# Kernel tuning notes

Measured on AMD Instinct MI355X. Metric: run time of the kernel, lower is better.

## Reference

```python
import jax, jax.numpy as jnp
import numpy as np


def setup_inputs() -> dict:
    key = jax.random.key(0)
    ks = jax.random.split(key, 16)
    B, P, ENC = 128, 196, 2048          # batch, num pixels (14x14), encoder feature size
    E = D = A = 512                      # embed, decoder(hidden), attention sizes
    V, L = 10000, 52                     # vocab, max caption length
    s = 0.02
    rn = lambda k, shp: jax.random.normal(k, shp, jnp.float32) * s
    return {
        "features": jax.random.normal(ks[0], (B, P, ENC), jnp.float32),
        "captions": jax.random.randint(ks[1], (B, L), 0, V),
        "caption_lengths": jax.random.randint(ks[2], (B, 1), 2, L + 1),
        "emb": jax.random.uniform(ks[3], (V, E), jnp.float32, -0.1, 0.1),
        "W_enc_att": rn(ks[4], (ENC, A)), "b_enc_att": jnp.zeros((A,), jnp.float32),
        "W_dec_att": rn(ks[5], (D, A)),   "b_dec_att": jnp.zeros((A,), jnp.float32),
        "w_full": rn(ks[6], (A,)),        "b_full": jnp.zeros((), jnp.float32),
        "W_h0": rn(ks[7], (ENC, D)),      "b_h0": jnp.zeros((D,), jnp.float32),
        "W_c0": rn(ks[8], (ENC, D)),      "b_c0": jnp.zeros((D,), jnp.float32),
        "W_beta": rn(ks[9], (D, ENC)),    "b_beta": jnp.zeros((ENC,), jnp.float32),
        "W_ih": rn(ks[10], (E + ENC, 4 * D)), "b_ih": jnp.zeros((4 * D,), jnp.float32),
        "W_hh": rn(ks[11], (D, 4 * D)),       "b_hh": jnp.zeros((4 * D,), jnp.float32),
        "W_fc": jax.random.uniform(ks[12], (D, V), jnp.float32, -0.1, 0.1),
        "b_fc": jnp.zeros((V,), jnp.float32),
    }


def reference(features, captions, caption_lengths, emb,
              W_enc_att, b_enc_att, W_dec_att, b_dec_att, w_full, b_full,
              W_h0, b_h0, W_c0, b_c0, W_beta, b_beta,
              W_ih, b_ih, W_hh, b_hh, W_fc, b_fc):
    lens = caption_lengths[:, 0]
    order = jnp.argsort(-lens)                       # sort descending by length (stable)
    features = features[order]
    captions = captions[order]
    decode_lengths = lens[order] - 1                 # [B]
    T = captions.shape[1] - 1                        # static max decode length

    emb_seq = emb[captions[:, :T]]                   # [B,T,E]
    eo = features.mean(axis=1)                       # [B,ENC]
    h = eo @ W_h0 + b_h0                             # [B,D]
    c = eo @ W_c0 + b_c0
    enc_proj = features @ W_enc_att + b_enc_att      # [B,P,A] (precomputed, h-independent)

    def step(carry, xs):
        h, c = carry
        t, e_t = xs                                  # e_t: [B,E]
        mask = (decode_lengths > t)[:, None].astype(h.dtype)  # rows still decoding
        dec_proj = h @ W_dec_att + b_dec_att         # [B,A]
        scores = jax.nn.relu(enc_proj + dec_proj[:, None, :]) @ w_full + b_full  # [B,P]
        alpha = jax.nn.softmax(scores, axis=-1)      # [B,P]
        attw = jnp.einsum('bp,bpe->be', alpha, features)       # attention-weighted enc
        gate = jax.nn.sigmoid(h @ W_beta + b_beta)   # [B,ENC]
        x = jnp.concatenate([e_t, gate * attw], axis=1)        # [B,E+ENC]
        gates = x @ W_ih + b_ih + h @ W_hh + b_hh    # [B,4D], torch LSTMCell order i,f,g,o
        i, f, g, o = jnp.split(gates, 4, axis=1)
        c_new = jax.nn.sigmoid(f) * c + jax.nn.sigmoid(i) * jnp.tanh(g)
        h_new = jax.nn.sigmoid(o) * jnp.tanh(c_new)
        preds = h_new @ W_fc + b_fc                  # dropout is identity in eval
        h = mask * h_new + (1.0 - mask) * h          # freeze finished rows
        c = mask * c_new + (1.0 - mask) * c
        return (h, c), (preds * mask, alpha * mask)

    (_, _), (preds, alphas) = jax.lax.scan(
        step, (h, c), (jnp.arange(T), jnp.swapaxes(emb_seq, 0, 1)))
    predictions = jnp.swapaxes(preds, 0, 1)          # [B,T,V]
    alphas = jnp.swapaxes(alphas, 0, 1)              # [B,T,P]
    return predictions, captions, decode_lengths, alphas
```

## Files before the change

### kernel.cpp

```cpp
#include <hip/hip_runtime.h>
#include <math.h>

#define NB 128
#define NP 196
#define NENC 2048
#define NE 512
#define ND 512
#define NA 512
#define NV 10000
#define NVPAD 10112
#define NL 52
#define NT 51
#define KXH2 2560

typedef unsigned short u16;
typedef __attribute__((ext_vector_type(8))) short bf16x8;
typedef __attribute__((ext_vector_type(8))) unsigned short u16x8;
typedef __attribute__((ext_vector_type(4))) float f32x4;

#define MFMA16 __builtin_amdgcn_mfma_f32_16x16x32_bf16

__device__ __forceinline__ float sigmoidf_(float v) { return 1.0f / (1.0f + __expf(-v)); }
__device__ __forceinline__ float b2f(u16 u) { return __uint_as_float(((unsigned int)u) << 16); }
__device__ __forceinline__ u16 f2b(float f) {
  unsigned int u = __float_as_uint(f);
  unsigned int r = (u + 0x7FFFu + ((u >> 16) & 1u)) >> 16;
  return (u16)r;
}

__global__ void kSort(const int* __restrict__ cap_len, const int* __restrict__ captions,
                      int* __restrict__ order, int* __restrict__ nact,
                      float* __restrict__ out_cap, float* __restrict__ out_dlen) {
  __shared__ int lens[NB];
  __shared__ int s_dl[NB];
  int tid = threadIdx.x;
  lens[tid] = cap_len[tid];
  __syncthreads();
  int li = lens[tid];
  int r = 0;
  for (int j = 0; j < NB; ++j) {
    int lj = lens[j];
    if (lj > li || (lj == li && j < tid)) r++;
  }
  order[r] = tid;
  s_dl[r] = li - 1;
  out_dlen[r] = (float)(li - 1);
  for (int l = 0; l < NL; ++l)
    out_cap[(size_t)r * NL + l] = (float)captions[(size_t)tid * NL + l];
  __syncthreads();
  if (tid < NT) {
    int cnt = 0;
    for (int j = 0; j < NB; ++j) cnt += (s_dl[j] > tid) ? 1 : 0;
    nact[tid] = cnt;
  }
}

__global__ void kAlphaZero(const int* __restrict__ nact, float* __restrict__ out_alph) {
  int t = blockIdx.x;
  int n0 = nact[t];
  int cnt = (NB - n0) * NP;
  for (int i = threadIdx.x; i < cnt; i += 256) {
    int b = n0 + i / NP;
    int p = i - (i / NP) * NP;
    out_alph[((size_t)b * NT + t) * NP + p] = 0.0f;
  }
}

__global__ void kFeats(const float* __restrict__ features, const int* __restrict__ order,
                       u16* __restrict__ featsb) {
  int p = blockIdx.x, b = blockIdx.y, tid = threadIdx.x;
  const float* src = features + ((size_t)order[b] * NP + p) * NENC + tid * 8;
  u16* dst = featsb + ((size_t)b * NP + p) * NENC + tid * 8;
  float4 v0 = *(const float4*)src;
  float4 v1 = *(const float4*)(src + 4);
  u16x8 o;
  o[0] = f2b(v0.x); o[1] = f2b(v0.y); o[2] = f2b(v0.z); o[3] = f2b(v0.w);
  o[4] = f2b(v1.x); o[5] = f2b(v1.y); o[6] = f2b(v1.z); o[7] = f2b(v1.w);
  *(u16x8*)dst = o;
}

__global__ void kTWenc(const float* __restrict__ W, u16* __restrict__ dst) {
  int n = blockIdx.x;
  for (int k = threadIdx.x; k < NENC; k += 256)
    dst[(size_t)n * NENC + k] = f2b(W[(size_t)k * NA + n]);
}
__global__ void kTdg(const float* __restrict__ Wdec, const float* __restrict__ Wbeta,
                     u16* __restrict__ dst) {
  int n = blockIdx.x;
  for (int k = threadIdx.x; k < ND; k += 256) {
    float v = (n < NA) ? Wdec[(size_t)k * NA + n] : Wbeta[(size_t)k * NENC + (n - NA)];
    dst[(size_t)n * ND + k] = f2b(v);
  }
}
__global__ void kTWihTop(const float* __restrict__ Wih, u16* __restrict__ dst) {
  int n = blockIdx.x;
  int col = (n & 3) * ND + (n >> 2);
  for (int k = threadIdx.x; k < NE; k += 256)
    dst[(size_t)n * NE + k] = f2b(Wih[(size_t)k * (4 * ND) + col]);
}
__global__ void kTifgo2(const float* __restrict__ Wih, const float* __restrict__ Whh,
                        u16* __restrict__ dst) {
  int n = blockIdx.x;
  int col = (n & 3) * ND + (n >> 2);
  for (int k = threadIdx.x; k < KXH2; k += 256) {
    float v = (k < NENC) ? Wih[(size_t)(NE + k) * (4 * ND) + col]
                         : Whh[(size_t)(k - NENC) * (4 * ND) + col];
    dst[(size_t)n * KXH2 + k] = f2b(v);
  }
}
__global__ void kTfc(const float* __restrict__ Wfc, u16* __restrict__ dst) {
  int n = blockIdx.x;
  for (int k = threadIdx.x; k < ND; k += 256) {
    float v = (n < NV) ? Wfc[(size_t)k * NV + n] : 0.0f;
    dst[(size_t)n * ND + k] = f2b(v);
  }
}

__global__ void kEmbA(const float* __restrict__ emb, const int* __restrict__ captions,
                      const int* __restrict__ order, u16* __restrict__ embA) {
  int t = blockIdx.x, b = blockIdx.y;
  int tok = captions[(size_t)order[b] * NL + t];
  int i = threadIdx.x * 2;
  float2 v = *(const float2*)(emb + (size_t)tok * NE + i);
  unsigned int w0 = (unsigned int)f2b(v.x) | ((unsigned int)f2b(v.y) << 16);
  *(unsigned int*)(embA + ((size_t)t * NB + b) * NE + i) = w0;
}

__global__ __launch_bounds__(256) void kEmbGemm(const u16* __restrict__ A,
                                                const u16* __restrict__ BT,
                                                u16* __restrict__ D) {
  int w = threadIdx.x >> 6, lane = threadIdx.x & 63;
  int lr = lane & 15, lg = lane >> 4;
  int mb = blockIdx.y * 128 + w * 32;
  int nb = blockIdx.x * 64;
  f32x4 acc[2][4] = {};
  const u16* a0 = A + (size_t)(mb + lr) * NE + lg * 8;
  const u16* a1 = a0 + 16 * NE;
  const u16* b0 = BT + (size_t)(nb + lr) * NE + lg * 8;
  for (int k0 = 0; k0 < NE; k0 += 32) {
    bf16x8 af0 = *(const bf16x8*)(a0 + k0);
    bf16x8 af1 = *(const bf16x8*)(a1 + k0);
#pragma unroll
    for (int nt = 0; nt < 4; ++nt) {
      bf16x8 bf = *(const bf16x8*)(b0 + (size_t)nt * 16 * NE + k0);
      acc[0][nt] = MFMA16(af0, bf, acc[0][nt], 0, 0, 0);
      acc[1][nt] = MFMA16(af1, bf, acc[1][nt], 0, 0, 0);
    }
  }
#pragma unroll
  for (int mt = 0; mt < 2; ++mt)
#pragma unroll
    for (int nt = 0; nt < 4; ++nt)
#pragma unroll
      for (int j = 0; j < 4; ++j) {
        int row = mb + mt * 16 + lg * 4 + j;
        int col = nb + nt * 16 + lr;
        D[(size_t)row * NENC + col] = f2b(acc[mt][nt][j]);
      }
}

__global__ void kEo(const u16* __restrict__ featsb, float* __restrict__ eo) {
  int e = blockIdx.x * 256 + threadIdx.x;
  int b = blockIdx.y;
  const u16* f = featsb + (size_t)b * NP * NENC + e;
  float s = 0.0f;
  for (int p = 0; p < NP; ++p) s += b2f(f[(size_t)p * NENC]);
  eo[(size_t)b * NENC + e] = s * (1.0f / NP);
}

__global__ void kInitHC(const float* __restrict__ eo,
                        const float* __restrict__ W_h0, const float* __restrict__ b_h0,
                        const float* __restrict__ W_c0, const float* __restrict__ b_c0,
                        u16* __restrict__ hb, u16* __restrict__ xh0, float* __restrict__ c) {
  __shared__ float s_eo[NENC];
  int b = blockIdx.y;
  for (int i = threadIdx.x; i < NENC; i += 256) s_eo[i] = eo[(size_t)b * NENC + i];
  __syncthreads();
  int d = blockIdx.x * 256 + threadIdx.x;
  const float* W = blockIdx.z ? W_c0 : W_h0;
  const float* bias = blockIdx.z ? b_c0 : b_h0;
  float acc = bias[d];
  for (int k = 0; k < NENC; ++k) acc += s_eo[k] * W[(size_t)k * ND + d];
  if (blockIdx.z) {
    c[(size_t)b * ND + d] = acc;
  } else {
    u16 hv = f2b(acc);
    hb[(size_t)b * ND + d] = hv;
    xh0[(size_t)b * KXH2 + NENC + d] = hv;
  }
}

__global__ __launch_bounds__(256) void kEncProj(const u16* __restrict__ A,
                                                const u16* __restrict__ BT,
                                                const float* __restrict__ bias,
                                                u16* __restrict__ D) {
  __shared__ u16 As[128][72];
  int bid = blockIdx.x;
  int mt = bid >> 2, ntile = bid & 3;
  int mb = mt * 128, nb = ntile * 128;
  int tid = threadIdx.x;
  int w = tid >> 6, lane = tid & 63;
  int lr = lane & 15, lg = lane >> 4;

  int arow[4], akp[4];
  const u16* aptr[4];
#pragma unroll
  for (int i = 0; i < 4; ++i) {
    int idx = i * 256 + tid;
    arow[i] = idx >> 3;
    akp[i] = idx & 7;
    aptr[i] = A + (size_t)(mb + arow[i]) * NENC + akp[i] * 8;
  }
  u16x8 stg0, stg1, stg2, stg3;
  stg0 = *(const u16x8*)(aptr[0]);
  stg1 = *(const u16x8*)(aptr[1]);
  stg2 = *(const u16x8*)(aptr[2]);
  stg3 = *(const u16x8*)(aptr[3]);

  f32x4 acc[2][8] = {};
  const u16* bbase = BT + (size_t)(nb + lr) * NENC + lg * 8;

  for (int k0 = 0; k0 < NENC; k0 += 64) {
    __syncthreads();
    *(u16x8*)&As[arow[0]][akp[0] * 8] = stg0;
    *(u16x8*)&As[arow[1]][akp[1] * 8] = stg1;
    *(u16x8*)&As[arow[2]][akp[2] * 8] = stg2;
    *(u16x8*)&As[arow[3]][akp[3] * 8] = stg3;
    if (k0 + 64 < NENC) {
      stg0 = *(const u16x8*)(aptr[0] + k0 + 64);
      stg1 = *(const u16x8*)(aptr[1] + k0 + 64);
      stg2 = *(const u16x8*)(aptr[2] + k0 + 64);
      stg3 = *(const u16x8*)(aptr[3] + k0 + 64);
    }
    __syncthreads();
#pragma unroll
    for (int kh = 0; kh < 2; ++kh) {
      int r0 = w * 32 + lr;
      bf16x8 af0 = *(const bf16x8*)&As[r0][kh * 32 + lg * 8];
      bf16x8 af1 = *(const bf16x8*)&As[r0 + 16][kh * 32 + lg * 8];
#pragma unroll
      for (int nt = 0; nt < 8; ++nt) {
        bf16x8 bf = *(const bf16x8*)(bbase + (size_t)nt * 16 * NENC + k0 + kh * 32);
        acc[0][nt] = MFMA16(af0, bf, acc[0][nt], 0, 0, 0);
        acc[1][nt] = MFMA16(af1, bf, acc[1][nt], 0, 0, 0);
      }
    }
  }
#pragma unroll
  for (int m2 = 0; m2 < 2; ++m2)
#pragma unroll
    for (int nt = 0; nt < 8; ++nt)
#pragma unroll
      for (int j = 0; j < 4; ++j) {
        int row = mb + w * 32 + m2 * 16 + lg * 4 + j;
        int col = nb + nt * 16 + lr;
        D[(size_t)row * NA + col] = f2b(acc[m2][nt][j] + bias[col]);
      }
}

__global__ __launch_bounds__(64) void kDecGate(const u16* __restrict__ hb,
                                               const u16* __restrict__ BT,
                                               const float* __restrict__ b_dec,
                                               const float* __restrict__ b_beta,
                                               const int* __restrict__ nact, int t,
                                               float* __restrict__ dec_proj,
                                               float* __restrict__ gate_raw) {
  int nact_t = nact[t];
  int mb = blockIdx.y * 32;
  if (mb >= nact_t) return;
  int lane = threadIdx.x;
  int lr = lane & 15, lg = lane >> 4;
  int nb = blockIdx.x * 32;
  f32x4 acc[2][2] = {};
  const u16* a0 = hb + (size_t)(mb + lr) * ND + lg * 8;
  const u16* a1 = a0 + 16 * ND;
  const u16* b0 = BT + (size_t)(nb + lr) * ND + lg * 8;
  const u16* b1 = b0 + 16 * ND;
#pragma unroll 4
  for (int k0 = 0; k0 < ND; k0 += 32) {
    bf16x8 af0 = *(const bf16x8*)(a0 + k0);
    bf16x8 af1 = *(const bf16x8*)(a1 + k0);
    bf16x8 bv0 = *(const bf16x8*)(b0 + k0);
    bf16x8 bv1 = *(const bf16x8*)(b1 + k0);
    acc[0][0] = MFMA16(af0, bv0, acc[0][0], 0, 0, 0);
    acc[1][0] = MFMA16(af1, bv0, acc[1][0], 0, 0, 0);
    acc[0][1] = MFMA16(af0, bv1, acc[0][1], 0, 0, 0);
    acc[1][1] = MFMA16(af1, bv1, acc[1][1], 0, 0, 0);
  }
#pragma unroll
  for (int mt = 0; mt < 2; ++mt)
#pragma unroll
    for (int nt = 0; nt < 2; ++nt)
#pragma unroll
      for (int j = 0; j < 4; ++j) {
        int row = mb + mt * 16 + lg * 4 + j;
        int n = nb + nt * 16 + lr;
        if (n < NA)
          dec_proj[(size_t)row * NA + n] = acc[mt][nt][j] + b_dec[n];
        else
          gate_raw[(size_t)row * NENC + (n - NA)] = acc[mt][nt][j] + b_beta[n - NA];
      }
}

__global__ __launch_bounds__(256) void kSAX(const u16* __restrict__ featsb,
                                            const u16* __restrict__ encb,
                                            const float* __restrict__ dec_proj,
                                            const float* __restrict__ gate_raw,
                                            const float* __restrict__ w_full,
                                            const float* __restrict__ b_full,
                                            const int* __restrict__ nact, int t,
                                            u16* __restrict__ xh_w,
                                            float* __restrict__ out_alph) {
  int b = blockIdx.x, r = blockIdx.y, tid = threadIdx.x;
  if (b >= nact[t]) return;
  __shared__ float s_dp[NA], s_wf[NA], s_al[NP + 12], red[16];
  for (int i = tid; i < NA; i += 256) { s_dp[i] = dec_proj[(size_t)b * NA + i]; s_wf[i] = w_full[i]; }
  __syncthreads();
  int wave = tid >> 6, lane = tid & 63;
  float bf_ = b_full[0];
  for (int p = wave; p < NP; p += 4) {
    const u16* ep = encb + ((size_t)b * NP + p) * NA + lane * 8;
    u16x8 v = *(const u16x8*)ep;
    float acc = 0.0f;
#pragma unroll
    for (int j = 0; j < 8; ++j) {
      int a = lane * 8 + j;
      float vv = b2f(v[j]) + s_dp[a];
      acc += fmaxf(vv, 0.0f) * s_wf[a];
    }
#pragma unroll
    for (int off = 32; off; off >>= 1) acc += __shfl_down(acc, off);
    if (lane == 0) s_al[p] = acc + bf_;
  }
  __syncthreads();
  float mx = -3.4e38f;
  for (int p = tid; p < NP; p += 256) mx = fmaxf(mx, s_al[p]);
#pragma unroll
  for (int off = 32; off; off >>= 1) mx = fmaxf(mx, __shfl_down(mx, off));
  if (lane == 0) red[wave] = mx;
  __syncthreads();
  if (tid == 0) red[0] = fmaxf(fmaxf(red[0], red[1]), fmaxf(red[2], red[3]));
  __syncthreads();
  float m2v = red[0];
  float sm = 0.0f;
  for (int p = tid; p < NP; p += 256) { float e = __expf(s_al[p] - m2v); s_al[p] = e; sm += e; }
#pragma unroll
  for (int off = 32; off; off >>= 1) sm += __shfl_down(sm, off);
  if (lane == 0) red[8 + wave] = sm;
  __syncthreads();
  if (tid == 0) red[8] = 1.0f / (red[8] + red[9] + red[10] + red[11]);
  __syncthreads();
  float inv = red[8];
  for (int p = tid; p < NP; p += 256) {
    float al = s_al[p] * inv;
    s_al[p] = al;
    if (r == 0) out_alph[((size_t)b * NT + t) * NP + p] = al;
  }
  __syncthreads();
  int e0 = r * 512 + tid * 2;
  float ac0 = 0.0f, ac1 = 0.0f;
  const u16* fb = featsb + (size_t)b * NP * NENC + e0;
#pragma unroll 4
  for (int p = 0; p < NP; ++p) {
    unsigned int v = *(const unsigned int*)(fb + (size_t)p * NENC);
    float al = s_al[p];
    ac0 += al * __uint_as_float(v << 16);
    ac1 += al * __uint_as_float(v & 0xffff0000u);
  }
  float g0 = sigmoidf_(gate_raw[(size_t)b * NENC + e0]);
  float g1 = sigmoidf_(gate_raw[(size_t)b * NENC + e0 + 1]);
  unsigned int wo = (unsigned int)f2b(ac0 * g0) | ((unsigned int)f2b(ac1 * g1) << 16);
  *(unsigned int*)(xh_w + (size_t)b * KXH2 + e0) = wo;
}

__global__ __launch_bounds__(1024) void kGatesLstm(const u16* __restrict__ xh_r,
                                                   const u16* __restrict__ WifgoT2,
                                                   const u16* __restrict__ embAll,
                                                   const float* __restrict__ b_ih,
                                                   const float* __restrict__ b_hh,
                                                   const int* __restrict__ nact, int t,
                                                   float* __restrict__ cst,
                                                   u16* __restrict__ hb,
                                                   u16* __restrict__ hnewAll_t,
                                                   u16* __restrict__ xh_w) {
  __shared__ float smem[8 * 32 * 33];
  int nact_t = nact[t];
  int tid = threadIdx.x;
  int w = tid >> 6, lane = tid & 63;
  int lr = lane & 15, lg = lane >> 4;
  int rt = blockIdx.x & 3, ct = blockIdx.x >> 2;
  int mb = rt * 32, nb = ct * 32;
  int kq = w >> 1, mh = w & 1;
  if (mb < nact_t) {
    f32x4 acc0 = {}, acc1 = {};
    const u16* pa = xh_r + (size_t)(mb + mh * 16 + lr) * KXH2 + kq * 320 + lg * 8;
    const u16* pb0 = WifgoT2 + (size_t)(nb + lr) * KXH2 + kq * 320 + lg * 8;
    const u16* pb1 = pb0 + (size_t)16 * KXH2;
#pragma unroll
    for (int k0 = 0; k0 < 320; k0 += 32) {
      bf16x8 af = *(const bf16x8*)(pa + k0);
      bf16x8 bv0 = *(const bf16x8*)(pb0 + k0);
      bf16x8 bv1 = *(const bf16x8*)(pb1 + k0);
      acc0 = MFMA16(af, bv0, acc0, 0, 0, 0);
      acc1 = MFMA16(af, bv1, acc1, 0, 0, 0);
    }
#pragma unroll
    for (int j = 0; j < 4; ++j) {
      int rr = kq * 32 + mh * 16 + lg * 4 + j;
      smem[rr * 33 + lr] = acc0[j];
      smem[rr * 33 + 16 + lr] = acc1[j];
    }
  }
  __syncthreads();
  if (tid < 256) {
    int row = tid >> 3, dl = tid & 7;
    int grow = mb + row;
    int d = ct * 8 + dl;
    size_t off = (size_t)grow * ND + d;
    if (grow < nact_t) {
      float g4[4];
#pragma unroll
      for (int g = 0; g < 4; ++g) {
        int col = dl * 4 + g;
        float s = 0.0f;
#pragma unroll
        for (int q = 0; q < 8; ++q) s += smem[(q * 32 + row) * 33 + col];
        s += b2f(embAll[((size_t)t * NB + grow) * NENC + nb + col]);
        g4[g] = s;
      }
      float gi = g4[0] + b_ih[d] + b_hh[d];
      float gf = g4[1] + b_ih[ND + d] + b_hh[ND + d];
      float gg = g4[2] + b_ih[2 * ND + d] + b_hh[2 * ND + d];
      float go = g4[3] + b_ih[3 * ND + d] + b_hh[3 * ND + d];
      float cn = sigmoidf_(gf) * cst[off] + sigmoidf_(gi) * tanhf(gg);
      float hn = sigmoidf_(go) * tanhf(cn);
      u16 hv = f2b(hn);
      cst[off] = cn;
      hb[off] = hv;
      hnewAll_t[off] = hv;
      xh_w[(size_t)grow * KXH2 + NENC + d] = hv;
    } else {
      xh_w[(size_t)grow * KXH2 + NENC + d] = hb[off];
    }
  }
}

__global__ __launch_bounds__(256) void kPredsAllT(const u16* __restrict__ hnewAll,
                                                  const u16* __restrict__ BT,
                                                  const float* __restrict__ b_fc,
                                                  const int* __restrict__ nact,
                                                  float* __restrict__ out_pred) {
  int nb = blockIdx.x * 64;
  int w = threadIdx.x >> 6, lane = threadIdx.x & 63;
  int lr = lane & 15, lg = lane >> 4;
  int mb = w * 32;
  const u16* b0 = BT + (size_t)(nb + lr) * ND + lg * 8;
#pragma unroll
  for (int ti = 0; ti < 4; ++ti) {
    int t = blockIdx.y * 4 + ti;
    if (t >= NT) break;
    int nact_t = nact[t];
    f32x4 acc[2][4] = {};
    if (mb < nact_t) {
      const u16* a0 = hnewAll + (size_t)t * NB * ND + (size_t)(mb + lr) * ND + lg * 8;
      const u16* a1 = a0 + 16 * ND;
      for (int k0 = 0; k0 < ND; k0 += 32) {
        bf16x8 af0 = *(const bf16x8*)(a0 + k0);
        bf16x8 af1 = *(const bf16x8*)(a1 + k0);
#pragma unroll
        for (int nt = 0; nt < 4; ++nt) {
          bf16x8 bf = *(const bf16x8*)(b0 + (size_t)nt * 16 * ND + k0);
          acc[0][nt] = MFMA16(af0, bf, acc[0][nt], 0, 0, 0);
          acc[1][nt] = MFMA16(af1, bf, acc[1][nt], 0, 0, 0);
        }
      }
    }
#pragma unroll
    for (int mt = 0; mt < 2; ++mt)
#pragma unroll
      for (int nt = 0; nt < 4; ++nt)
#pragma unroll
        for (int j = 0; j < 4; ++j) {
          int gn = nb + nt * 16 + lr;
          if (gn < NV) {
            int row = mb + mt * 16 + lg * 4 + j;
            float v = (row < nact_t) ? (acc[mt][nt][j] + b_fc[gn]) : 0.0f;
            __builtin_nontemporal_store(v, &out_pred[((size_t)row * NT + t) * NV + gn]);
          }
        }
  }
}

extern "C" void kernel_launch(void* const* d_in, const int* in_sizes, int n_in,
                              void* d_out, int out_size, void* d_ws, size_t ws_size,
                              hipStream_t stream) {
  (void)in_sizes; (void)n_in; (void)out_size; (void)ws_size;
  const float* features  = (const float*)d_in[0];
  const int*   captions  = (const int*)d_in[1];
  const int*   cap_len   = (const int*)d_in[2];
  const float* emb       = (const float*)d_in[3];
  const float* W_enc_att = (const float*)d_in[4];
  const float* b_enc_att = (const float*)d_in[5];
  const float* W_dec_att = (const float*)d_in[6];
  const float* b_dec_att = (const float*)d_in[7];
  const float* w_full    = (const float*)d_in[8];
  const float* b_full    = (const float*)d_in[9];
  const float* W_h0      = (const float*)d_in[10];
  const float* b_h0      = (const float*)d_in[11];
  const float* W_c0      = (const float*)d_in[12];
  const float* b_c0      = (const float*)d_in[13];
  const float* W_beta    = (const float*)d_in[14];
  const float* b_beta    = (const float*)d_in[15];
  const float* W_ih      = (const float*)d_in[16];
  const float* b_ih      = (const float*)d_in[17];
  const float* W_hh      = (const float*)d_in[18];
  const float* b_hh      = (const float*)d_in[19];
  const float* W_fc      = (const float*)d_in[20];
  const float* b_fc      = (const float*)d_in[21];

  float* out      = (float*)d_out;
  float* out_pred = out;
  float* out_cap  = out_pred + (size_t)NB * NT * NV;
  float* out_dlen = out_cap + (size_t)NB * NL;
  float* out_alph = out_dlen + NB;

  char* p = (char*)d_ws;
  auto alloc = [&](size_t nbytes) { void* r = (void*)p; p += (nbytes + 255) & ~(size_t)255; return r; };
  int*   order    = (int*)alloc(NB * 4);
  int*   nact     = (int*)alloc(NT * 4);
  float* eo       = (float*)alloc((size_t)NB * NENC * 4);
  float* c        = (float*)alloc((size_t)NB * ND * 4);
  u16*   hb       = (u16*)alloc((size_t)NB * ND * 2);
  u16*   xh0      = (u16*)alloc((size_t)NB * KXH2 * 2);
  u16*   xh1      = (u16*)alloc((size_t)NB * KXH2 * 2);
  u16*   hnewAll  = (u16*)alloc((size_t)NT * NB * ND * 2);
  float* dec_proj = (float*)alloc((size_t)NB * NA * 4);
  float* gate_raw = (float*)alloc((size_t)NB * NENC * 4);
  u16*   featsb   = (u16*)alloc((size_t)NB * NP * NENC * 2);
  u16*   encb     = (u16*)alloc((size_t)NB * NP * NA * 2);
  u16*   WencT    = (u16*)alloc((size_t)NA * NENC * 2);
  u16*   WdgT     = (u16*)alloc((size_t)(NA + NENC) * ND * 2);
  u16*   WihTopT  = (u16*)alloc((size_t)NENC * NE * 2);
  u16*   WifgoT2  = (u16*)alloc((size_t)NENC * KXH2 * 2);
  u16*   WfcT     = (u16*)alloc((size_t)NVPAD * ND * 2);
  u16*   embA     = (u16*)alloc((size_t)NT * NB * NE * 2);
  u16*   embAll   = (u16*)alloc((size_t)NT * NB * NENC * 2);

  kSort<<<1, NB, 0, stream>>>(cap_len, captions, order, nact, out_cap, out_dlen);
  kAlphaZero<<<NT, 256, 0, stream>>>(nact, out_alph);
  kFeats<<<dim3(NP, NB), 256, 0, stream>>>(features, order, featsb);
  kTWenc<<<NA, 256, 0, stream>>>(W_enc_att, WencT);
  kTdg<<<NA + NENC, 256, 0, stream>>>(W_dec_att, W_beta, WdgT);
  kTWihTop<<<NENC, 256, 0, stream>>>(W_ih, WihTopT);
  kTifgo2<<<NENC, 256, 0, stream>>>(W_ih, W_hh, WifgoT2);
  kTfc<<<NVPAD, 256, 0, stream>>>(W_fc, WfcT);
  kEmbA<<<dim3(NT, NB), 256, 0, stream>>>(emb, captions, order, embA);
  kEmbGemm<<<dim3(NENC / 64, NT), 256, 0, stream>>>(embA, WihTopT, embAll);
  kEo<<<dim3(NENC / 256, NB), 256, 0, stream>>>(featsb, eo);
  kInitHC<<<dim3(ND / 256, NB, 2), 256, 0, stream>>>(eo, W_h0, b_h0, W_c0, b_c0, hb, xh0, c);
  kEncProj<<<784, 256, 0, stream>>>(featsb, WencT, b_enc_att, encb);

  for (int t = 0; t < NT; ++t) {
    u16* xh_r = (t & 1) ? xh1 : xh0;
    u16* xh_w = (t & 1) ? xh0 : xh1;
    kDecGate<<<dim3((NA + NENC) / 32, 4), 64, 0, stream>>>(hb, WdgT, b_dec_att, b_beta,
                                                           nact, t, dec_proj, gate_raw);
    kSAX<<<dim3(NB, 4), 256, 0, stream>>>(featsb, encb, dec_proj, gate_raw, w_full, b_full,
                                          nact, t, xh_r, out_alph);
    kGatesLstm<<<256, 1024, 0, stream>>>(xh_r, WifgoT2, embAll, b_ih, b_hh, nact, t,
                                         c, hb, hnewAll + (size_t)t * NB * ND, xh_w);
  }
  kPredsAllT<<<dim3(NVPAD / 64, (NT + 3) / 4), 256, 0, stream>>>(hnewAll, WfcT, b_fc, nact, out_pred);
}
```

Before: 4.618 ms.

## Tile weight transposes, MFMA init-state GEMM, double-buffer enc proj, reshape preds grid

The separate per-row weight transpose kernels become one LDS-tiled transpose kernel with coalesced reads and vectorised writes. The scalar fp32 h0/c0 initialisation becomes a bf16 MFMA GEMM against a new transposed combined W_h0/W_c0 matrix. The encoder projection GEMM double-buffers its LDS A tile so each k-step needs one barrier instead of two. The prediction kernel launches one block per timestep and vocab tile instead of looping over four timesteps, which gives more blocks. The cost is extra workspace and bf16 rounding of the mean feature vector and of the init weights.

```diff
diff --git a/kernel.cpp b/kernel.cpp
--- a/kernel.cpp
+++ b/kernel.cpp
@@ -79,41 +79,43 @@
   *(u16x8*)dst = o;
 }
 
-__global__ void kTWenc(const float* __restrict__ W, u16* __restrict__ dst) {
-  int n = blockIdx.x;
-  for (int k = threadIdx.x; k < NENC; k += 256)
-    dst[(size_t)n * NENC + k] = f2b(W[(size_t)k * NA + n]);
-}
-__global__ void kTdg(const float* __restrict__ Wdec, const float* __restrict__ Wbeta,
-                     u16* __restrict__ dst) {
-  int n = blockIdx.x;
-  for (int k = threadIdx.x; k < ND; k += 256) {
-    float v = (n < NA) ? Wdec[(size_t)k * NA + n] : Wbeta[(size_t)k * NENC + (n - NA)];
-    dst[(size_t)n * ND + k] = f2b(v);
-  }
-}
-__global__ void kTWihTop(const float* __restrict__ Wih, u16* __restrict__ dst) {
-  int n = blockIdx.x;
-  int col = (n & 3) * ND + (n >> 2);
-  for (int k = threadIdx.x; k < NE; k += 256)
-    dst[(size_t)n * NE + k] = f2b(Wih[(size_t)k * (4 * ND) + col]);
-}
-__global__ void kTifgo2(const float* __restrict__ Wih, const float* __restrict__ Whh,
-                        u16* __restrict__ dst) {
-  int n = blockIdx.x;
-  int col = (n & 3) * ND + (n >> 2);
-  for (int k = threadIdx.x; k < KXH2; k += 256) {
-    float v = (k < NENC) ? Wih[(size_t)(NE + k) * (4 * ND) + col]
-                         : Whh[(size_t)(k - NENC) * (4 * ND) + col];
-    dst[(size_t)n * KXH2 + k] = f2b(v);
-  }
-}
-__global__ void kTfc(const float* __restrict__ Wfc, u16* __restrict__ dst) {
-  int n = blockIdx.x;
-  for (int k = threadIdx.x; k < ND; k += 256) {
-    float v = (n < NV) ? Wfc[(size_t)k * NV + n] : 0.0f;
-    dst[(size_t)n * ND + k] = f2b(v);
-  }
+__device__ __forceinline__ float tfetch(int mode, int k, int n,
+                                        const float* __restrict__ A,
+                                        const float* __restrict__ B) {
+  switch (mode) {
+    case 0: return A[(size_t)k * NA + n];
+    case 1: return (n < NA) ? A[(size_t)k * NA + n] : B[(size_t)k * NENC + (n - NA)];
+    case 2: return A[(size_t)k * (4 * ND) + (n & 3) * ND + (n >> 2)];
+    case 3: {
+      int col = (n & 3) * ND + (n >> 2);
+      return (k < NENC) ? A[(size_t)(NE + k) * (4 * ND) + col]
+                        : B[(size_t)(k - NENC) * (4 * ND) + col];
+    }
+    case 4: return (n < NV) ? A[(size_t)k * NV + n] : 0.0f;
+    default: return (n < NA) ? A[(size_t)k * ND + n] : B[(size_t)k * ND + (n - NA)];
+  }
+}
+
+__global__ __launch_bounds__(256) void kTrans(const float* __restrict__ A,
+                                              const float* __restrict__ B,
+                                              u16* __restrict__ dst,
+                                              int K, int N, int mode) {
+  __shared__ u16 T[32][136];
+  int n0 = blockIdx.x * 32, k0 = blockIdx.y * 128;
+  int tid = threadIdx.x;
+  int c = tid & 31, kr = tid >> 5;
+#pragma unroll
+  for (int pass = 0; pass < 16; ++pass) {
+    int kl = pass * 8 + kr;
+    T[c][kl] = f2b(tfetch(mode, k0 + kl, n0 + c, A, B));
+  }
+  __syncthreads();
+  int row = tid >> 3, seg = tid & 7;
+  u16x8 v0, v1;
+#pragma unroll
+  for (int j = 0; j < 8; ++j) { v0[j] = T[row][seg * 16 + j]; v1[j] = T[row][seg * 16 + 8 + j]; }
+  *(u16x8*)&dst[(size_t)(n0 + row) * K + k0 + seg * 16] = v0;
+  *(u16x8*)&dst[(size_t)(n0 + row) * K + k0 + seg * 16 + 8] = v1;
 }
 
 __global__ void kEmbA(const float* __restrict__ emb, const int* __restrict__ captions,
@@ -159,42 +161,63 @@
       }
 }
 
-__global__ void kEo(const u16* __restrict__ featsb, float* __restrict__ eo) {
+__global__ void kEo(const u16* __restrict__ featsb, u16* __restrict__ eob) {
   int e = blockIdx.x * 256 + threadIdx.x;
   int b = blockIdx.y;
   const u16* f = featsb + (size_t)b * NP * NENC + e;
   float s = 0.0f;
   for (int p = 0; p < NP; ++p) s += b2f(f[(size_t)p * NENC]);
-  eo[(size_t)b * NENC + e] = s * (1.0f / NP);
-}
-
-__global__ void kInitHC(const float* __restrict__ eo,
-                        const float* __restrict__ W_h0, const float* __restrict__ b_h0,
-                        const float* __restrict__ W_c0, const float* __restrict__ b_c0,
-                        u16* __restrict__ hb, u16* __restrict__ xh0, float* __restrict__ c) {
-  __shared__ float s_eo[NENC];
-  int b = blockIdx.y;
-  for (int i = threadIdx.x; i < NENC; i += 256) s_eo[i] = eo[(size_t)b * NENC + i];
-  __syncthreads();
-  int d = blockIdx.x * 256 + threadIdx.x;
-  const float* W = blockIdx.z ? W_c0 : W_h0;
-  const float* bias = blockIdx.z ? b_c0 : b_h0;
-  float acc = bias[d];
-  for (int k = 0; k < NENC; ++k) acc += s_eo[k] * W[(size_t)k * ND + d];
-  if (blockIdx.z) {
-    c[(size_t)b * ND + d] = acc;
-  } else {
-    u16 hv = f2b(acc);
-    hb[(size_t)b * ND + d] = hv;
-    xh0[(size_t)b * KXH2 + NENC + d] = hv;
-  }
+  eob[(size_t)b * NENC + e] = f2b(s * (1.0f / NP));
+}
+
+__global__ __launch_bounds__(64) void kHC0(const u16* __restrict__ eob,
+                                           const u16* __restrict__ BT,
+                                           const float* __restrict__ b_h0,
+                                           const float* __restrict__ b_c0,
+                                           u16* __restrict__ hb, u16* __restrict__ xh0,
+                                           float* __restrict__ c) {
+  int lane = threadIdx.x;
+  int lr = lane & 15, lg = lane >> 4;
+  int mb = blockIdx.y * 32, nb = blockIdx.x * 32;
+  f32x4 acc[2][2] = {};
+  const u16* a0 = eob + (size_t)(mb + lr) * NENC + lg * 8;
+  const u16* a1 = a0 + 16 * NENC;
+  const u16* b0 = BT + (size_t)(nb + lr) * NENC + lg * 8;
+  const u16* b1 = b0 + 16 * NENC;
+#pragma unroll 4
+  for (int k0 = 0; k0 < NENC; k0 += 32) {
+    bf16x8 af0 = *(const bf16x8*)(a0 + k0);
+    bf16x8 af1 = *(const bf16x8*)(a1 + k0);
+    bf16x8 bv0 = *(const bf16x8*)(b0 + k0);
+    bf16x8 bv1 = *(const bf16x8*)(b1 + k0);
+    acc[0][0] = MFMA16(af0, bv0, acc[0][0], 0, 0, 0);
+    acc[1][0] = MFMA16(af1, bv0, acc[1][0], 0, 0, 0);
+    acc[0][1] = MFMA16(af0, bv1, acc[0][1], 0, 0, 0);
+    acc[1][1] = MFMA16(af1, bv1, acc[1][1], 0, 0, 0);
+  }
+#pragma unroll
+  for (int mt = 0; mt < 2; ++mt)
+#pragma unroll
+    for (int nt = 0; nt < 2; ++nt)
+#pragma unroll
+      for (int j = 0; j < 4; ++j) {
+        int row = mb + mt * 16 + lg * 4 + j;
+        int n = nb + nt * 16 + lr;
+        if (n < NA) {
+          u16 hv = f2b(acc[mt][nt][j] + b_h0[n]);
+          hb[(size_t)row * ND + n] = hv;
+          xh0[(size_t)row * KXH2 + NENC + n] = hv;
+        } else {
+          c[(size_t)row * ND + (n - NA)] = acc[mt][nt][j] + b_c0[n - NA];
+        }
+      }
 }
 
 __global__ __launch_bounds__(256) void kEncProj(const u16* __restrict__ A,
                                                 const u16* __restrict__ BT,
                                                 const float* __restrict__ bias,
                                                 u16* __restrict__ D) {
-  __shared__ u16 As[128][72];
+  __shared__ u16 As[2][128][72];
   int bid = blockIdx.x;
   int mt = bid >> 2, ntile = bid & 3;
   int mb = mt * 128, nb = ntile * 128;
@@ -211,33 +234,33 @@
     akp[i] = idx & 7;
     aptr[i] = A + (size_t)(mb + arow[i]) * NENC + akp[i] * 8;
   }
-  u16x8 stg0, stg1, stg2, stg3;
-  stg0 = *(const u16x8*)(aptr[0]);
-  stg1 = *(const u16x8*)(aptr[1]);
-  stg2 = *(const u16x8*)(aptr[2]);
-  stg3 = *(const u16x8*)(aptr[3]);
+  u16x8 s0 = *(const u16x8*)(aptr[0]);
+  u16x8 s1 = *(const u16x8*)(aptr[1]);
+  u16x8 s2 = *(const u16x8*)(aptr[2]);
+  u16x8 s3 = *(const u16x8*)(aptr[3]);
+  *(u16x8*)&As[0][arow[0]][akp[0] * 8] = s0;
+  *(u16x8*)&As[0][arow[1]][akp[1] * 8] = s1;
+  *(u16x8*)&As[0][arow[2]][akp[2] * 8] = s2;
+  *(u16x8*)&As[0][arow[3]][akp[3] * 8] = s3;
 
   f32x4 acc[2][8] = {};
   const u16* bbase = BT + (size_t)(nb + lr) * NENC + lg * 8;
+  int cur = 0;
+  int r0 = w * 32 + lr;
 
   for (int k0 = 0; k0 < NENC; k0 += 64) {
     __syncthreads();
-    *(u16x8*)&As[arow[0]][akp[0] * 8] = stg0;
-    *(u16x8*)&As[arow[1]][akp[1] * 8] = stg1;
-    *(u16x8*)&As[arow[2]][akp[2] * 8] = stg2;
-    *(u16x8*)&As[arow[3]][akp[3] * 8] = stg3;
-    if (k0 + 64 < NENC) {
-      stg0 = *(const u16x8*)(aptr[0] + k0 + 64);
-      stg1 = *(const u16x8*)(aptr[1] + k0 + 64);
-      stg2 = *(const u16x8*)(aptr[2] + k0 + 64);
-      stg3 = *(const u16x8*)(aptr[3] + k0 + 64);
-    }
-    __syncthreads();
+    bool more = (k0 + 64 < NENC);
+    if (more) {
+      s0 = *(const u16x8*)(aptr[0] + k0 + 64);
+      s1 = *(const u16x8*)(aptr[1] + k0 + 64);
+      s2 = *(const u16x8*)(aptr[2] + k0 + 64);
+      s3 = *(const u16x8*)(aptr[3] + k0 + 64);
+    }
 #pragma unroll
     for (int kh = 0; kh < 2; ++kh) {
-      int r0 = w * 32 + lr;
-      bf16x8 af0 = *(const bf16x8*)&As[r0][kh * 32 + lg * 8];
-      bf16x8 af1 = *(const bf16x8*)&As[r0 + 16][kh * 32 + lg * 8];
+      bf16x8 af0 = *(const bf16x8*)&As[cur][r0][kh * 32 + lg * 8];
+      bf16x8 af1 = *(const bf16x8*)&As[cur][r0 + 16][kh * 32 + lg * 8];
 #pragma unroll
       for (int nt = 0; nt < 8; ++nt) {
         bf16x8 bf = *(const bf16x8*)(bbase + (size_t)nt * 16 * NENC + k0 + kh * 32);
@@ -245,6 +268,13 @@
         acc[1][nt] = MFMA16(af1, bf, acc[1][nt], 0, 0, 0);
       }
     }
+    if (more) {
+      *(u16x8*)&As[cur ^ 1][arow[0]][akp[0] * 8] = s0;
+      *(u16x8*)&As[cur ^ 1][arow[1]][akp[1] * 8] = s1;
+      *(u16x8*)&As[cur ^ 1][arow[2]][akp[2] * 8] = s2;
+      *(u16x8*)&As[cur ^ 1][arow[3]][akp[3] * 8] = s3;
+    }
+    cur ^= 1;
   }
 #pragma unroll
   for (int m2 = 0; m2 < 2; ++m2)
@@ -445,50 +475,46 @@
   }
 }
 
-__global__ __launch_bounds__(256) void kPredsAllT(const u16* __restrict__ hnewAll,
+__global__ __launch_bounds__(256) void kPredsAll2(const u16* __restrict__ hnewAll,
                                                   const u16* __restrict__ BT,
                                                   const float* __restrict__ b_fc,
                                                   const int* __restrict__ nact,
                                                   float* __restrict__ out_pred) {
-  int nb = blockIdx.x * 64;
+  int t = blockIdx.x;
+  int nb = blockIdx.y * 64;
+  int nact_t = nact[t];
   int w = threadIdx.x >> 6, lane = threadIdx.x & 63;
   int lr = lane & 15, lg = lane >> 4;
   int mb = w * 32;
-  const u16* b0 = BT + (size_t)(nb + lr) * ND + lg * 8;
-#pragma unroll
-  for (int ti = 0; ti < 4; ++ti) {
-    int t = blockIdx.y * 4 + ti;
-    if (t >= NT) break;
-    int nact_t = nact[t];
-    f32x4 acc[2][4] = {};
-    if (mb < nact_t) {
-      const u16* a0 = hnewAll + (size_t)t * NB * ND + (size_t)(mb + lr) * ND + lg * 8;
-      const u16* a1 = a0 + 16 * ND;
-      for (int k0 = 0; k0 < ND; k0 += 32) {
-        bf16x8 af0 = *(const bf16x8*)(a0 + k0);
-        bf16x8 af1 = *(const bf16x8*)(a1 + k0);
-#pragma unroll
-        for (int nt = 0; nt < 4; ++nt) {
-          bf16x8 bf = *(const bf16x8*)(b0 + (size_t)nt * 16 * ND + k0);
-          acc[0][nt] = MFMA16(af0, bf, acc[0][nt], 0, 0, 0);
-          acc[1][nt] = MFMA16(af1, bf, acc[1][nt], 0, 0, 0);
+  f32x4 acc[2][4] = {};
+  if (mb < nact_t) {
+    const u16* a0 = hnewAll + (size_t)t * NB * ND + (size_t)(mb + lr) * ND + lg * 8;
+    const u16* a1 = a0 + 16 * ND;
+    const u16* b0 = BT + (size_t)(nb + lr) * ND + lg * 8;
+    for (int k0 = 0; k0 < ND; k0 += 32) {
+      bf16x8 af0 = *(const bf16x8*)(a0 + k0);
+      bf16x8 af1 = *(const bf16x8*)(a1 + k0);
+#pragma unroll
+      for (int nt = 0; nt < 4; ++nt) {
+        bf16x8 bf = *(const bf16x8*)(b0 + (size_t)nt * 16 * ND + k0);
+        acc[0][nt] = MFMA16(af0, bf, acc[0][nt], 0, 0, 0);
+        acc[1][nt] = MFMA16(af1, bf, acc[1][nt], 0, 0, 0);
+      }
+    }
+  }
+#pragma unroll
+  for (int mt = 0; mt < 2; ++mt)
+#pragma unroll
+    for (int nt = 0; nt < 4; ++nt)
+#pragma unroll
+      for (int j = 0; j < 4; ++j) {
+        int gn = nb + nt * 16 + lr;
+        if (gn < NV) {
+          int row = mb + mt * 16 + lg * 4 + j;
+          float v = (row < nact_t) ? (acc[mt][nt][j] + b_fc[gn]) : 0.0f;
+          __builtin_nontemporal_store(v, &out_pred[((size_t)row * NT + t) * NV + gn]);
         }
       }
-    }
-#pragma unroll
-    for (int mt = 0; mt < 2; ++mt)
-#pragma unroll
-      for (int nt = 0; nt < 4; ++nt)
-#pragma unroll
-        for (int j = 0; j < 4; ++j) {
-          int gn = nb + nt * 16 + lr;
-          if (gn < NV) {
-            int row = mb + mt * 16 + lg * 4 + j;
-            float v = (row < nact_t) ? (acc[mt][nt][j] + b_fc[gn]) : 0.0f;
-            __builtin_nontemporal_store(v, &out_pred[((size_t)row * NT + t) * NV + gn]);
-          }
-        }
-  }
 }
 
 extern "C" void kernel_launch(void* const* d_in, const int* in_sizes, int n_in,
@@ -528,7 +554,7 @@
   auto alloc = [&](size_t nbytes) { void* r = (void*)p; p += (nbytes + 255) & ~(size_t)255; return r; };
   int*   order    = (int*)alloc(NB * 4);
   int*   nact     = (int*)alloc(NT * 4);
-  float* eo       = (float*)alloc((size_t)NB * NENC * 4);
+  u16*   eob      = (u16*)alloc((size_t)NB * NENC * 2);
   float* c        = (float*)alloc((size_t)NB * ND * 4);
   u16*   hb       = (u16*)alloc((size_t)NB * ND * 2);
   u16*   xh0      = (u16*)alloc((size_t)NB * KXH2 * 2);
@@ -543,21 +569,23 @@
   u16*   WihTopT  = (u16*)alloc((size_t)NENC * NE * 2);
   u16*   WifgoT2  = (u16*)alloc((size_t)NENC * KXH2 * 2);
   u16*   WfcT     = (u16*)alloc((size_t)NVPAD * ND * 2);
+  u16*   WhcT     = (u16*)alloc((size_t)1024 * NENC * 2);
   u16*   embA     = (u16*)alloc((size_t)NT * NB * NE * 2);
   u16*   embAll   = (u16*)alloc((size_t)NT * NB * NENC * 2);
 
   kSort<<<1, NB, 0, stream>>>(cap_len, captions, order, nact, out_cap, out_dlen);
   kAlphaZero<<<NT, 256, 0, stream>>>(nact, out_alph);
   kFeats<<<dim3(NP, NB), 256, 0, stream>>>(features, order, featsb);
-  kTWenc<<<NA, 256, 0, stream>>>(W_enc_att, WencT);
-  kTdg<<<NA + NENC, 256, 0, stream>>>(W_dec_att, W_beta, WdgT);
-  kTWihTop<<<NENC, 256, 0, stream>>>(W_ih, WihTopT);
-  kTifgo2<<<NENC, 256, 0, stream>>>(W_ih, W_hh, WifgoT2);
-  kTfc<<<NVPAD, 256, 0, stream>>>(W_fc, WfcT);
+  kTrans<<<dim3(512 / 32, 2048 / 128), 256, 0, stream>>>(W_enc_att, nullptr, WencT, 2048, 512, 0);
+  kTrans<<<dim3(2560 / 32, 512 / 128), 256, 0, stream>>>(W_dec_att, W_beta, WdgT, 512, 2560, 1);
+  kTrans<<<dim3(2048 / 32, 512 / 128), 256, 0, stream>>>(W_ih, nullptr, WihTopT, 512, 2048, 2);
+  kTrans<<<dim3(2048 / 32, 2560 / 128), 256, 0, stream>>>(W_ih, W_hh, WifgoT2, 2560, 2048, 3);
+  kTrans<<<dim3(NVPAD / 32, 512 / 128), 256, 0, stream>>>(W_fc, nullptr, WfcT, 512, NVPAD, 4);
+  kTrans<<<dim3(1024 / 32, 2048 / 128), 256, 0, stream>>>(W_h0, W_c0, WhcT, 2048, 1024, 5);
   kEmbA<<<dim3(NT, NB), 256, 0, stream>>>(emb, captions, order, embA);
   kEmbGemm<<<dim3(NENC / 64, NT), 256, 0, stream>>>(embA, WihTopT, embAll);
-  kEo<<<dim3(NENC / 256, NB), 256, 0, stream>>>(featsb, eo);
-  kInitHC<<<dim3(ND / 256, NB, 2), 256, 0, stream>>>(eo, W_h0, b_h0, W_c0, b_c0, hb, xh0, c);
+  kEo<<<dim3(NENC / 256, NB), 256, 0, stream>>>(featsb, eob);
+  kHC0<<<dim3(1024 / 32, NB / 32), 64, 0, stream>>>(eob, WhcT, b_h0, b_c0, hb, xh0, c);
   kEncProj<<<784, 256, 0, stream>>>(featsb, WencT, b_enc_att, encb);
 
   for (int t = 0; t < NT; ++t) {
@@ -570,5 +598,5 @@
     kGatesLstm<<<256, 1024, 0, stream>>>(xh_r, WifgoT2, embAll, b_ih, b_hh, nact, t,
                                          c, hb, hnewAll + (size_t)t * NB * ND, xh_w);
   }
-  kPredsAllT<<<dim3(NVPAD / 64, (NT + 3) / 4), 256, 0, stream>>>(hnewAll, WfcT, b_fc, nact, out_pred);
-}
+  kPredsAll2<<<dim3(NT, NVPAD / 64), 256, 0, stream>>>(hnewAll, WfcT, b_fc, nact, out_pred);
+}
```

Result: faster. 4.508 ms (-2.4%).
